# Optimization experiments

Measured on AMD Instinct MI355X. Metric: run time of the kernel, lower is better.

## Reference

```python
import jax, jax.numpy as jnp
import numpy as np

TOP_K = 2


def setup_inputs() -> dict:
    key = jax.random.key(0)
    k1, k2, k3, k4, k5 = jax.random.split(key, 5)
    H, F, E = 1024, 2048, 8
    B, S = 2, 1024
    return {
        "hidden_states": jax.random.normal(k1, (B, S, H), dtype=jnp.float32),
        "gate_w": jax.random.normal(k2, (E, H), dtype=jnp.float32) * (1.0 / np.sqrt(H)),
        "w1": jax.random.normal(k3, (E, F, H), dtype=jnp.float32) * (1.0 / np.sqrt(H)),
        "w2": jax.random.normal(k4, (E, H, F), dtype=jnp.float32) * (1.0 / np.sqrt(F)),
        "w3": jax.random.normal(k5, (E, F, H), dtype=jnp.float32) * (1.0 / np.sqrt(H)),
    }


def reference(hidden_states, gate_w, w1, w2, w3):
    B, S, H = hidden_states.shape
    E = gate_w.shape[0]
    x = hidden_states.reshape(-1, H)  # [T, H]

    # Router: softmax in float32, top-k, renormalize (exact Mixtral math)
    router_logits = x @ gate_w.T  # [T, E]
    probs = jax.nn.softmax(router_logits.astype(jnp.float32), axis=-1)
    routing_weights, selected = jax.lax.top_k(probs, TOP_K)  # [T, K]
    routing_weights = routing_weights / routing_weights.sum(axis=-1, keepdims=True)
    routing_weights = routing_weights.astype(x.dtype)

    # Per-token combine weight for each expert: [T, E]
    combine = (jax.nn.one_hot(selected, E, dtype=x.dtype) * routing_weights[..., None]).sum(axis=1)

    # Dense grouped expert SwiGLU MLP (zero combine weight for unselected experts
    # makes this strictly equivalent to the gathered/dispatched computation)
    h = jnp.einsum('th,efh->etf', x, w1)   # [E, T, F]
    g = jnp.einsum('th,efh->etf', x, w3)   # [E, T, F]
    mid = jax.nn.silu(h) * g               # SwiGLU
    expert_out = jnp.einsum('etf,ehf->eth', mid, w2)  # [E, T, H]
    out = jnp.einsum('eth,te->th', expert_out, combine)  # weighted combine

    return out.reshape(B, S, H), router_logits
```

## Files before the change

kernel.cpp:

```cpp
#include <hip/hip_runtime.h>
#include <hip/hip_bf16.h>
#include <math.h>

#define H 1024
#define FF 2048
#define E 8
#define T 2048
#define NSLOT (2*T)
#define SLOT_PAD 128

#define XCONV_BLKS 512
#define ROUTER_BLKS T
#define K1_BLKS (XCONV_BLKS + ROUTER_BLKS)

typedef __attribute__((ext_vector_type(8))) short s16x8;
typedef __attribute__((ext_vector_type(4))) float f32x4;
typedef __attribute__((ext_vector_type(4))) unsigned int u32x4;

static __device__ __forceinline__ unsigned short f2bf(float f) {
    union { float f; unsigned u; } v; v.f = f;
    unsigned r = v.u + 0x7fff + ((v.u >> 16) & 1);
    return (unsigned short)(r >> 16);
}
static __device__ __forceinline__ float bf2f(unsigned short s) {
    union { unsigned u; float f; } v; v.u = ((unsigned)s) << 16;
    return v.f;
}
static __device__ __forceinline__ unsigned pack2(float a, float b) {
    return (unsigned)f2bf(a) | ((unsigned)f2bf(b) << 16);
}

typedef __attribute__((address_space(3))) unsigned int lds_uint;
typedef const __attribute__((address_space(1))) unsigned int glob_uint;
static __device__ __forceinline__ void gl_lds16(const void* g, void* l) {
    __builtin_amdgcn_global_load_lds((glob_uint*)g, (lds_uint*)l, 16, 0, 0);
}

static __device__ __forceinline__ void expert_range(const int* __restrict__ counts,
                                                    int e, int& off, int& cnt) {
    int acc = 0;
    #pragma unroll
    for (int i = 0; i < E; ++i) {
        int c = counts[i];
        if (i < e) acc += c;
        if (i == e) cnt = c;
    }
    off = acc;
}

static __device__ __forceinline__ u32x4 pack8(f32x4 a, f32x4 b) {
    u32x4 r;
    r.x = pack2(a.x, a.y); r.y = pack2(a.z, a.w);
    r.z = pack2(b.x, b.y); r.w = pack2(b.z, b.w);
    return r;
}

__global__ __launch_bounds__(256) void prep_kernel(
    const float* __restrict__ x, const float* __restrict__ gw,
    unsigned short* __restrict__ xb,
    float* __restrict__ logits_out, int* __restrict__ top_id,
    float* __restrict__ top_w, int* __restrict__ counts)
{
    int b = blockIdx.x;
    int tid = threadIdx.x;
    if (b < XCONV_BLKS) {
        size_t base = (size_t)b * 4096;
        size_t i0 = base + (size_t)(0 * 256 + tid) * 4;
        size_t i1 = base + (size_t)(1 * 256 + tid) * 4;
        size_t i2 = base + (size_t)(2 * 256 + tid) * 4;
        size_t i3 = base + (size_t)(3 * 256 + tid) * 4;
        f32x4 a0 = *(const f32x4*)(x + i0);
        f32x4 a1 = *(const f32x4*)(x + i1);
        f32x4 a2 = *(const f32x4*)(x + i2);
        f32x4 a3 = *(const f32x4*)(x + i3);
        uint2 r0, r1, r2, r3;
        r0.x = pack2(a0.x, a0.y); r0.y = pack2(a0.z, a0.w);
        r1.x = pack2(a1.x, a1.y); r1.y = pack2(a1.z, a1.w);
        r2.x = pack2(a2.x, a2.y); r2.y = pack2(a2.z, a2.w);
        r3.x = pack2(a3.x, a3.y); r3.y = pack2(a3.z, a3.w);
        *(uint2*)(xb + i0) = r0;
        *(uint2*)(xb + i1) = r1;
        *(uint2*)(xb + i2) = r2;
        *(uint2*)(xb + i3) = r3;
        return;
    }
    int t = b - XCONV_BLKS;
    int e = tid >> 5;
    int l32 = tid & 31;
    const float* xr = x + (size_t)t * H;
    const float* gr = gw + (size_t)e * H;
    float s = 0.f;
    for (int h = l32; h < H; h += 32) s += xr[h] * gr[h];
    for (int off = 16; off; off >>= 1) s += __shfl_down(s, off, 32);
    __shared__ float lg[E];
    if (l32 == 0) lg[e] = s;
    __syncthreads();
    if (tid < E) logits_out[(size_t)t * E + tid] = lg[tid];
    if (tid == 0) {
        int i1 = 0; float b1 = lg[0];
        for (int i = 1; i < E; ++i) if (lg[i] > b1) { b1 = lg[i]; i1 = i; }
        int i2 = -1; float b2 = -INFINITY;
        for (int i = 0; i < E; ++i) if (i != i1 && lg[i] > b2) { b2 = lg[i]; i2 = i; }
        float p2 = expf(b2 - b1);
        float inv = 1.f / (1.f + p2);
        top_id[2*t]   = i1;  top_id[2*t+1] = i2;
        top_w[2*t]    = inv; top_w[2*t+1]  = p2 * inv;
        atomicAdd(&counts[i1], 1);
        atomicAdd(&counts[i2], 1);
    }
}

__global__ __launch_bounds__(256) void assign_kernel(
    const int* __restrict__ top_id, const int* __restrict__ counts,
    int* __restrict__ cursors, int* __restrict__ top_pos,
    int* __restrict__ slot_token)
{
    int t = blockIdx.x * 256 + threadIdx.x;
    if (t >= T) return;
    int offs[E];
    {
        int acc = 0;
        #pragma unroll
        for (int i = 0; i < E; ++i) { offs[i] = acc; acc += counts[i]; }
    }
    #pragma unroll
    for (int k = 0; k < 2; ++k) {
        int e = top_id[2*t + k];
        int p = offs[e] + atomicAdd(&cursors[e], 1);
        top_pos[2*t + k] = p;
        slot_token[p] = t;
    }
}

__global__ __launch_bounds__(256) void gemm1_kernel(
    const unsigned short* __restrict__ xb, const int* __restrict__ slot_token,
    const float* __restrict__ w1f, const float* __restrict__ w3f,
    const int* __restrict__ counts, unsigned short* __restrict__ mid)
{
    int e = blockIdx.z;
    int off, cnt;
    expert_range(counts, e, off, cnt);
    int m0 = blockIdx.y * 128;
    if (m0 >= cnt) return;
    int f0 = blockIdx.x * 64;

    __shared__ __align__(16) unsigned short sx[128 * 64];
    __shared__ __align__(16) unsigned short s1[64 * 64];
    __shared__ __align__(16) unsigned short s3[64 * 64];

    int tid = threadIdx.x;
    int wv = tid >> 6, ln = tid & 63;
    int quad = ln >> 4, l16 = ln & 15;
    int wm = wv & 1, wn = wv >> 1;
    int xor7 = l16 & 7;

    const unsigned short* xsrc[4]; unsigned short* xdst[4];
    #pragma unroll
    for (int j = 0; j < 4; ++j) {
        int row = wv * 32 + j * 8 + (ln >> 3);
        int slot = off + m0 + row;
        if (m0 + row >= cnt) slot = off;
        int tok = slot_token[slot];
        int cl = (ln & 7) ^ (row & 7);
        xsrc[j] = xb + (size_t)tok * H + cl * 8;
        xdst[j] = &sx[(wv * 32 + j * 8) * 64];
    }
    const float* w1s[2]; const float* w3s[2]; int bdst[2];
    #pragma unroll
    for (int h = 0; h < 2; ++h) {
        int slot = h * 256 + tid;
        int row = slot >> 3;
        int g = slot & 7;
        w1s[h] = w1f + ((size_t)e * FF + f0 + row) * H + g * 8;
        w3s[h] = w3f + ((size_t)e * FF + f0 + row) * H + g * 8;
        bdst[h] = row * 64 + ((g ^ (row & 7)) << 3);
    }

    f32x4 acc1[4][2], acc3[4][2];
    #pragma unroll
    for (int i = 0; i < 4; ++i)
        #pragma unroll
        for (int j = 0; j < 2; ++j) {
            acc1[i][j] = (f32x4){0.f, 0.f, 0.f, 0.f};
            acc3[i][j] = (f32x4){0.f, 0.f, 0.f, 0.f};
        }

    for (int k0 = 0; k0 < H; k0 += 64) {
        #pragma unroll
        for (int j = 0; j < 4; ++j) gl_lds16(xsrc[j] + k0, xdst[j]);
        #pragma unroll
        for (int h = 0; h < 2; ++h) {
            f32x4 u0 = *(const f32x4*)(w1s[h] + k0);
            f32x4 u1 = *(const f32x4*)(w1s[h] + k0 + 4);
            f32x4 v0 = *(const f32x4*)(w3s[h] + k0);
            f32x4 v1 = *(const f32x4*)(w3s[h] + k0 + 4);
            *(u32x4*)&s1[bdst[h]] = pack8(u0, u1);
            *(u32x4*)&s3[bdst[h]] = pack8(v0, v1);
        }
        __syncthreads();
        #pragma unroll
        for (int ks = 0; ks < 2; ++ks) {
            int cph = ((quad + 4 * ks) ^ xor7) << 3;
            s16x8 a[4], b1v[2], b3v[2];
            #pragma unroll
            for (int i = 0; i < 4; ++i)
                a[i] = *(const s16x8*)&sx[(wm * 64 + i * 16 + l16) * 64 + cph];
            #pragma unroll
            for (int j = 0; j < 2; ++j) {
                b1v[j] = *(const s16x8*)&s1[(wn * 32 + j * 16 + l16) * 64 + cph];
                b3v[j] = *(const s16x8*)&s3[(wn * 32 + j * 16 + l16) * 64 + cph];
            }
            #pragma unroll
            for (int i = 0; i < 4; ++i)
                #pragma unroll
                for (int j = 0; j < 2; ++j) {
                    acc1[i][j] = __builtin_amdgcn_mfma_f32_16x16x32_bf16(a[i], b1v[j], acc1[i][j], 0, 0, 0);
                    acc3[i][j] = __builtin_amdgcn_mfma_f32_16x16x32_bf16(a[i], b3v[j], acc3[i][j], 0, 0, 0);
                }
        }
        __syncthreads();
    }

    #pragma unroll
    for (int i = 0; i < 4; ++i) {
        #pragma unroll
        for (int r = 0; r < 4; ++r) {
            int row = wm * 64 + i * 16 + quad * 4 + r;
            if (m0 + row < cnt) {
                size_t base = (size_t)(off + m0 + row) * FF + f0 + wn * 32;
                #pragma unroll
                for (int j = 0; j < 2; ++j) {
                    float h = acc1[i][j][r];
                    float g = acc3[i][j][r];
                    float v = h / (1.f + __expf(-h)) * g;
                    mid[base + j * 16 + l16] = f2bf(v);
                }
            }
        }
    }
}

__global__ __launch_bounds__(256) void gemm2_kernel(
    const unsigned short* __restrict__ mid, const float* __restrict__ w2f,
    const int* __restrict__ counts, unsigned short* __restrict__ y)
{
    int e = blockIdx.z;
    int off, cnt;
    expert_range(counts, e, off, cnt);
    int m0 = blockIdx.y * 128;
    if (m0 >= cnt) return;
    int n0 = blockIdx.x * 64;

    __shared__ __align__(16) unsigned short sa[128 * 64];
    __shared__ __align__(16) unsigned short sb[64 * 64];

    int tid = threadIdx.x;
    int wv = tid >> 6, ln = tid & 63;
    int quad = ln >> 4, l16 = ln & 15;
    int wm = wv & 1, wn = wv >> 1;
    int xor7 = l16 & 7;

    const unsigned short* asrc[4]; unsigned short* adst[4];
    #pragma unroll
    for (int j = 0; j < 4; ++j) {
        int row = wv * 32 + j * 8 + (ln >> 3);
        int cl = (ln & 7) ^ (row & 7);
        asrc[j] = mid + (size_t)(off + m0 + row) * FF + cl * 8;
        adst[j] = &sa[(wv * 32 + j * 8) * 64];
    }
    const float* w2s[2]; int bdst[2];
    #pragma unroll
    for (int h = 0; h < 2; ++h) {
        int slot = h * 256 + tid;
        int row = slot >> 3;
        int g = slot & 7;
        w2s[h] = w2f + ((size_t)e * H + n0 + row) * FF + g * 8;
        bdst[h] = row * 64 + ((g ^ (row & 7)) << 3);
    }

    f32x4 acc[4][2];
    #pragma unroll
    for (int i = 0; i < 4; ++i)
        #pragma unroll
        for (int j = 0; j < 2; ++j) acc[i][j] = (f32x4){0.f, 0.f, 0.f, 0.f};

    for (int k0 = 0; k0 < FF; k0 += 64) {
        #pragma unroll
        for (int j = 0; j < 4; ++j) gl_lds16(asrc[j] + k0, adst[j]);
        #pragma unroll
        for (int h = 0; h < 2; ++h) {
            f32x4 u0 = *(const f32x4*)(w2s[h] + k0);
            f32x4 u1 = *(const f32x4*)(w2s[h] + k0 + 4);
            *(u32x4*)&sb[bdst[h]] = pack8(u0, u1);
        }
        __syncthreads();
        #pragma unroll
        for (int ks = 0; ks < 2; ++ks) {
            int cph = ((quad + 4 * ks) ^ xor7) << 3;
            s16x8 a[4], b[2];
            #pragma unroll
            for (int i = 0; i < 4; ++i)
                a[i] = *(const s16x8*)&sa[(wm * 64 + i * 16 + l16) * 64 + cph];
            #pragma unroll
            for (int j = 0; j < 2; ++j)
                b[j] = *(const s16x8*)&sb[(wn * 32 + j * 16 + l16) * 64 + cph];
            #pragma unroll
            for (int i = 0; i < 4; ++i)
                #pragma unroll
                for (int j = 0; j < 2; ++j)
                    acc[i][j] = __builtin_amdgcn_mfma_f32_16x16x32_bf16(a[i], b[j], acc[i][j], 0, 0, 0);
        }
        __syncthreads();
    }

    #pragma unroll
    for (int i = 0; i < 4; ++i) {
        #pragma unroll
        for (int r = 0; r < 4; ++r) {
            int row = wm * 64 + i * 16 + quad * 4 + r;
            if (m0 + row < cnt) {
                size_t base = (size_t)(off + m0 + row) * H + n0 + wn * 32;
                #pragma unroll
                for (int j = 0; j < 2; ++j)
                    y[base + j * 16 + l16] = f2bf(acc[i][j][r]);
            }
        }
    }
}

__global__ __launch_bounds__(256) void combine_kernel(
    const unsigned short* __restrict__ y, const int* __restrict__ top_pos,
    const float* __restrict__ top_w, float* __restrict__ out)
{
    int t = blockIdx.x, tid = threadIdx.x;
    int p0 = top_pos[2*t], p1 = top_pos[2*t+1];
    float w0 = top_w[2*t], w1 = top_w[2*t+1];
    ushort4 a = ((const ushort4*)(y + (size_t)p0 * H))[tid];
    ushort4 b = ((const ushort4*)(y + (size_t)p1 * H))[tid];
    float4 o;
    o.x = w0 * bf2f(a.x) + w1 * bf2f(b.x);
    o.y = w0 * bf2f(a.y) + w1 * bf2f(b.y);
    o.z = w0 * bf2f(a.z) + w1 * bf2f(b.z);
    o.w = w0 * bf2f(a.w) + w1 * bf2f(b.w);
    ((float4*)(out + (size_t)t * H))[tid] = o;
}

extern "C" void kernel_launch(void* const* d_in, const int* in_sizes, int n_in,
                              void* d_out, int out_size, void* d_ws, size_t ws_size,
                              hipStream_t stream) {
    const float* x  = (const float*)d_in[0];
    const float* gw = (const float*)d_in[1];
    const float* w1 = (const float*)d_in[2];
    const float* w2 = (const float*)d_in[3];
    const float* w3 = (const float*)d_in[4];
    float* out    = (float*)d_out;
    float* logits = out + (size_t)T * H;

    int* counts      = (int*)d_ws;
    int* cursors     = counts + 8;
    int* top_id      = counts + 16;
    int* top_pos     = top_id + 2*T;
    int* slot_token  = top_pos + 2*T;
    float* top_w     = (float*)(slot_token + NSLOT);
    unsigned short* xb  = (unsigned short*)(top_w + 2*T);
    unsigned short* mid = xb  + (size_t)T * H;
    unsigned short* y   = mid + (size_t)(NSLOT + SLOT_PAD) * FF;

    (void)hipMemsetAsync(counts, 0, 16 * sizeof(int), stream);

    prep_kernel<<<K1_BLKS, 256, 0, stream>>>(x, gw, xb,
                                             logits, top_id, top_w, counts);
    assign_kernel<<<(T + 255) / 256, 256, 0, stream>>>(top_id, counts, cursors,
                                                       top_pos, slot_token);
    gemm1_kernel<<<dim3(FF / 64, 16, E), 256, 0, stream>>>(xb, slot_token,
                                                           w1, w3, counts, mid);
    gemm2_kernel<<<dim3(H / 64, 16, E), 256, 0, stream>>>(mid, w2, counts, y);
    combine_kernel<<<T, 256, 0, stream>>>(y, top_pos, top_w, out);
}
```

Before: 416.6 us.

## Double-buffer LDS tiles in both expert GEMMs to overlap loads with MFMA

Both expert GEMM kernels now keep two LDS buffers for the activation and weight tiles. The next K-slice is fetched (async global-to-LDS for activations, register prefetch for fp32 weights) before the MFMAs on the current slice run, and the converted weights are written to the other buffer afterwards. This removes one barrier per iteration and hides global-load latency behind compute. In exchange it doubles LDS use, to about 64KB in gemm1, which may cut occupancy, and it raises register pressure from the prefetched fp32 values.

After: 398.6 us. 1.05x faster.

```diff
diff --git a/kernel.cpp b/kernel.cpp
--- a/kernel.cpp
+++ b/kernel.cpp
@@ -144,9 +144,9 @@
     if (m0 >= cnt) return;
     int f0 = blockIdx.x * 64;
 
-    __shared__ __align__(16) unsigned short sx[128 * 64];
-    __shared__ __align__(16) unsigned short s1[64 * 64];
-    __shared__ __align__(16) unsigned short s3[64 * 64];
+    __shared__ __align__(16) unsigned short sx[2][128 * 64];
+    __shared__ __align__(16) unsigned short s1[2][64 * 64];
+    __shared__ __align__(16) unsigned short s3[2][64 * 64];
 
     int tid = threadIdx.x;
     int wv = tid >> 6, ln = tid & 63;
@@ -154,7 +154,7 @@
     int wm = wv & 1, wn = wv >> 1;
     int xor7 = l16 & 7;
 
-    const unsigned short* xsrc[4]; unsigned short* xdst[4];
+    const unsigned short* xsrc[4]; int xoff[4];
     #pragma unroll
     for (int j = 0; j < 4; ++j) {
         int row = wv * 32 + j * 8 + (ln >> 3);
@@ -163,7 +163,7 @@
         int tok = slot_token[slot];
         int cl = (ln & 7) ^ (row & 7);
         xsrc[j] = xb + (size_t)tok * H + cl * 8;
-        xdst[j] = &sx[(wv * 32 + j * 8) * 64];
+        xoff[j] = (wv * 32 + j * 8) * 64;
     }
     const float* w1s[2]; const float* w3s[2]; int bdst[2];
     #pragma unroll
@@ -185,30 +185,46 @@
             acc3[i][j] = (f32x4){0.f, 0.f, 0.f, 0.f};
         }
 
+    #pragma unroll
+    for (int j = 0; j < 4; ++j) gl_lds16(xsrc[j], &sx[0][xoff[j]]);
+    #pragma unroll
+    for (int h = 0; h < 2; ++h) {
+        f32x4 u0 = *(const f32x4*)(w1s[h]);
+        f32x4 u1 = *(const f32x4*)(w1s[h] + 4);
+        f32x4 v0 = *(const f32x4*)(w3s[h]);
+        f32x4 v1 = *(const f32x4*)(w3s[h] + 4);
+        *(u32x4*)&s1[0][bdst[h]] = pack8(u0, u1);
+        *(u32x4*)&s3[0][bdst[h]] = pack8(v0, v1);
+    }
+    __syncthreads();
+
+    int cur = 0;
     for (int k0 = 0; k0 < H; k0 += 64) {
-        #pragma unroll
-        for (int j = 0; j < 4; ++j) gl_lds16(xsrc[j] + k0, xdst[j]);
-        #pragma unroll
-        for (int h = 0; h < 2; ++h) {
-            f32x4 u0 = *(const f32x4*)(w1s[h] + k0);
-            f32x4 u1 = *(const f32x4*)(w1s[h] + k0 + 4);
-            f32x4 v0 = *(const f32x4*)(w3s[h] + k0);
-            f32x4 v1 = *(const f32x4*)(w3s[h] + k0 + 4);
-            *(u32x4*)&s1[bdst[h]] = pack8(u0, u1);
-            *(u32x4*)&s3[bdst[h]] = pack8(v0, v1);
-        }
-        __syncthreads();
+        int nxt = cur ^ 1;
+        bool pf = (k0 + 64 < H);
+        f32x4 pu0[2], pu1[2], pv0[2], pv1[2];
+        if (pf) {
+            #pragma unroll
+            for (int j = 0; j < 4; ++j) gl_lds16(xsrc[j] + k0 + 64, &sx[nxt][xoff[j]]);
+            #pragma unroll
+            for (int h = 0; h < 2; ++h) {
+                pu0[h] = *(const f32x4*)(w1s[h] + k0 + 64);
+                pu1[h] = *(const f32x4*)(w1s[h] + k0 + 68);
+                pv0[h] = *(const f32x4*)(w3s[h] + k0 + 64);
+                pv1[h] = *(const f32x4*)(w3s[h] + k0 + 68);
+            }
+        }
         #pragma unroll
         for (int ks = 0; ks < 2; ++ks) {
             int cph = ((quad + 4 * ks) ^ xor7) << 3;
             s16x8 a[4], b1v[2], b3v[2];
             #pragma unroll
             for (int i = 0; i < 4; ++i)
-                a[i] = *(const s16x8*)&sx[(wm * 64 + i * 16 + l16) * 64 + cph];
+                a[i] = *(const s16x8*)&sx[cur][(wm * 64 + i * 16 + l16) * 64 + cph];
             #pragma unroll
             for (int j = 0; j < 2; ++j) {
-                b1v[j] = *(const s16x8*)&s1[(wn * 32 + j * 16 + l16) * 64 + cph];
-                b3v[j] = *(const s16x8*)&s3[(wn * 32 + j * 16 + l16) * 64 + cph];
+                b1v[j] = *(const s16x8*)&s1[cur][(wn * 32 + j * 16 + l16) * 64 + cph];
+                b3v[j] = *(const s16x8*)&s3[cur][(wn * 32 + j * 16 + l16) * 64 + cph];
             }
             #pragma unroll
             for (int i = 0; i < 4; ++i)
@@ -218,7 +234,15 @@
                     acc3[i][j] = __builtin_amdgcn_mfma_f32_16x16x32_bf16(a[i], b3v[j], acc3[i][j], 0, 0, 0);
                 }
         }
+        if (pf) {
+            #pragma unroll
+            for (int h = 0; h < 2; ++h) {
+                *(u32x4*)&s1[nxt][bdst[h]] = pack8(pu0[h], pu1[h]);
+                *(u32x4*)&s3[nxt][bdst[h]] = pack8(pv0[h], pv1[h]);
+            }
+        }
         __syncthreads();
+        cur = nxt;
     }
 
     #pragma unroll
@@ -251,8 +275,8 @@
     if (m0 >= cnt) return;
     int n0 = blockIdx.x * 64;
 
-    __shared__ __align__(16) unsigned short sa[128 * 64];
-    __shared__ __align__(16) unsigned short sb[64 * 64];
+    __shared__ __align__(16) unsigned short sa[2][128 * 64];
+    __shared__ __align__(16) unsigned short sb[2][64 * 64];
 
     int tid = threadIdx.x;
     int wv = tid >> 6, ln = tid & 63;
@@ -260,13 +284,13 @@
     int wm = wv & 1, wn = wv >> 1;
     int xor7 = l16 & 7;
 
-    const unsigned short* asrc[4]; unsigned short* adst[4];
+    const unsigned short* asrc[4]; int aoff[4];
     #pragma unroll
     for (int j = 0; j < 4; ++j) {
         int row = wv * 32 + j * 8 + (ln >> 3);
         int cl = (ln & 7) ^ (row & 7);
         asrc[j] = mid + (size_t)(off + m0 + row) * FF + cl * 8;
-        adst[j] = &sa[(wv * 32 + j * 8) * 64];
+        aoff[j] = (wv * 32 + j * 8) * 64;
     }
     const float* w2s[2]; int bdst[2];
     #pragma unroll
@@ -284,33 +308,53 @@
         #pragma unroll
         for (int j = 0; j < 2; ++j) acc[i][j] = (f32x4){0.f, 0.f, 0.f, 0.f};
 
+    #pragma unroll
+    for (int j = 0; j < 4; ++j) gl_lds16(asrc[j], &sa[0][aoff[j]]);
+    #pragma unroll
+    for (int h = 0; h < 2; ++h) {
+        f32x4 u0 = *(const f32x4*)(w2s[h]);
+        f32x4 u1 = *(const f32x4*)(w2s[h] + 4);
+        *(u32x4*)&sb[0][bdst[h]] = pack8(u0, u1);
+    }
+    __syncthreads();
+
+    int cur = 0;
     for (int k0 = 0; k0 < FF; k0 += 64) {
-        #pragma unroll
-        for (int j = 0; j < 4; ++j) gl_lds16(asrc[j] + k0, adst[j]);
-        #pragma unroll
-        for (int h = 0; h < 2; ++h) {
-            f32x4 u0 = *(const f32x4*)(w2s[h] + k0);
-            f32x4 u1 = *(const f32x4*)(w2s[h] + k0 + 4);
-            *(u32x4*)&sb[bdst[h]] = pack8(u0, u1);
-        }
-        __syncthreads();
+        int nxt = cur ^ 1;
+        bool pf = (k0 + 64 < FF);
+        f32x4 pu0[2], pu1[2];
+        if (pf) {
+            #pragma unroll
+            for (int j = 0; j < 4; ++j) gl_lds16(asrc[j] + k0 + 64, &sa[nxt][aoff[j]]);
+            #pragma unroll
+            for (int h = 0; h < 2; ++h) {
+                pu0[h] = *(const f32x4*)(w2s[h] + k0 + 64);
+                pu1[h] = *(const f32x4*)(w2s[h] + k0 + 68);
+            }
+        }
         #pragma unroll
         for (int ks = 0; ks < 2; ++ks) {
             int cph = ((quad + 4 * ks) ^ xor7) << 3;
             s16x8 a[4], b[2];
             #pragma unroll
             for (int i = 0; i < 4; ++i)
-                a[i] = *(const s16x8*)&sa[(wm * 64 + i * 16 + l16) * 64 + cph];
+                a[i] = *(const s16x8*)&sa[cur][(wm * 64 + i * 16 + l16) * 64 + cph];
             #pragma unroll
             for (int j = 0; j < 2; ++j)
-                b[j] = *(const s16x8*)&sb[(wn * 32 + j * 16 + l16) * 64 + cph];
+                b[j] = *(const s16x8*)&sb[cur][(wn * 32 + j * 16 + l16) * 64 + cph];
             #pragma unroll
             for (int i = 0; i < 4; ++i)
                 #pragma unroll
                 for (int j = 0; j < 2; ++j)
                     acc[i][j] = __builtin_amdgcn_mfma_f32_16x16x32_bf16(a[i], b[j], acc[i][j], 0, 0, 0);
         }
+        if (pf) {
+            #pragma unroll
+            for (int h = 0; h < 2; ++h)
+                *(u32x4*)&sb[nxt][bdst[h]] = pack8(pu0[h], pu1[h]);
+        }
         __syncthreads();
+        cur = nxt;
     }
 
     #pragma unroll
```
